# Performance work log

Hardware: AMD Instinct MI355X
Metric: run time of the kernel (lower is better)

Reference implementation:

```python
import jax, jax.numpy as jnp
import numpy as np
from jax import lax

COND, PRED, DH, NOUT = 64, 32, 128, 1
M, LQ, N, LR = 8, 256, 64, 512


def setup_inputs() -> dict:
    key = jax.random.key(0)
    ks = jax.random.split(key, 8)
    g = lambda k, sh, s=0.05: jax.random.normal(k, sh, jnp.float32) * s
    return {
        "query": jax.random.normal(ks[0], (M, LQ), jnp.float32),
        "ref": jax.random.normal(ks[1], (N, LR), jnp.float32),
        "q_weight": g(ks[2], (DH, 1, COND)),
        "q_bias": jnp.zeros((DH,), jnp.float32),
        "k_weight": g(ks[3], (DH, 1, COND)),
        "k_bias": jnp.zeros((DH,), jnp.float32),
        "v_weight": g(ks[4], (DH, 1, PRED), 0.1),
        "v_bias": jnp.zeros((DH,), jnp.float32),
        "m_weight": jnp.full((NOUT, 1, COND), 1.0 / COND, jnp.float32),
        "m_bias": jnp.zeros((NOUT,), jnp.float32),
        "o_weight": g(ks[5], (NOUT * PRED, DH), 0.1),
        "o_bias": jnp.zeros((NOUT * PRED,), jnp.float32),
        "m_key": g(ks[6], (1, 1, DH), 1.0),
    }


DN = ('NCH', 'OIH', 'NCH')


def _minmax_conv(x, w, b, offset=None, scale=None):
    # x: [B,1,L], w: [H,1,k] -> y: [B,H,W]. Each length-k window is min-max
    # normalized before the conv contraction. Since offset/scale are constant
    # per window: conv((x-off)/sc) = (conv(x) - off*sum(w)) / sc.
    k = w.shape[-1]
    if offset is None:
        offset = lax.reduce_window(x, jnp.inf, lax.min, (1, 1, k), (1, 1, 1), 'VALID')
    if scale is None:
        mx = lax.reduce_window(x, -jnp.inf, lax.max, (1, 1, k), (1, 1, 1), 'VALID')
        scale = mx - offset
        scale = jnp.where(scale == 0.0, 1.0, scale)
    raw = lax.conv_general_dilated(x, w, (1,), 'VALID', dimension_numbers=DN)
    wsum = w.sum(axis=(1, 2))
    y = (raw - offset * wsum[None, :, None]) / scale + b[None, :, None]
    return y, offset, scale


def reference(query, ref, q_weight, q_bias, k_weight, k_bias, v_weight, v_bias,
              m_weight, m_bias, o_weight, o_bias, m_key):
    cond, pred = q_weight.shape[-1], v_weight.shape[-1]
    # ---- query encoding ----
    q_in = jnp.cumsum(query, axis=1)[:, None, :]
    q, q_off, q_scale = _minmax_conv(q_in, q_weight, q_bias)
    q = q.transpose(0, 2, 1)                   # [M,Q,H]
    Qn = q.shape[1]
    q_scale_t = q_scale.transpose(0, 2, 1)     # [M,Q,1]
    qp = jnp.pad(query, ((0, 0), (cond - 1, 0)))[:, None, :]
    mc = lax.conv_general_dilated(qp, m_weight, (1,), 'VALID', dimension_numbers=DN)
    mc = mc + m_bias[None, :, None]
    mc = mc[..., cond - pred:]                 # [M,NOUT,Q+pred-1]
    widx = jnp.arange(pred)[:, None] + jnp.arange(Qn)[None, :]
    mwin = mc[..., widx]                       # [M,NOUT,pred,Q]
    m = mwin.reshape(mwin.shape[0], -1, Qn).transpose(0, 2, 1)  # [M,Q,NOUT*pred]
    m = m / q_scale_t
    # ---- key / value encoding ----
    k_in = jnp.cumsum(ref, axis=1)[:, None, :-pred]
    k, k_off, k_scale = _minmax_conv(k_in, k_weight, k_bias)
    k = k.transpose(0, 2, 1)                   # [N,K,H]
    v_in = ref[:, None, cond:]
    v, _, _ = _minmax_conv(v_in, v_weight, v_bias,
                           offset=jnp.zeros_like(k_off), scale=k_scale)
    v = v.transpose(0, 2, 1)                   # [N,K,H]
    # ---- scores ----
    full_score = jnp.einsum('mqh,nkh->mqkn', q, k)           # [M,Q,K,N]
    m_score = jnp.sum(q * m_key, axis=-1, keepdims=True)     # [M,Q,1]
    # ---- semi-hard attention: top-1 window per reference series ----
    ref_score = full_score.max(axis=2)         # [M,Q,N]
    max_idx = full_score.argmax(axis=2)        # [M,Q,N]
    n_ids = jnp.arange(v.shape[0])[None, None, :]
    sel_v = v[n_ids, max_idx]                  # [M,Q,N,H]
    sel_v = sel_v @ o_weight.T + o_bias        # [M,Q,N,D]
    scores = jax.nn.softmax(jnp.concatenate([ref_score, m_score], axis=-1), axis=-1)
    rs, ms = scores[..., :-1], scores[..., -1:]
    p = jnp.einsum('mqn,mqnd->mqd', rs, sel_v) + ms * m      # [M,Q,D]
    return p * q_scale_t
```

## Files before the change

kernel.cpp:

```cpp
#include <hip/hip_runtime.h>
#include <cmath>

#define M_B   8
#define LQ    256
#define N_B   64
#define LR    512
#define COND  64
#define PRED  32
#define DH    128
#define QN    193
#define KN    417
#define QPAD  256
#define KPAD  448
#define QROWS 1544
#define QGRPS 49

typedef _Float16 half8 __attribute__((ext_vector_type(8)));
typedef float f32x16 __attribute__((ext_vector_type(16)));

__device__ __forceinline__ f32x16 mfma_f16(half8 a, half8 b, f32x16 c) {
    return __builtin_amdgcn_mfma_f32_32x32x16_f16(a, b, c, 0, 0, 0);
}
__device__ __forceinline__ f32x16 zero16() {
    f32x16 z;
    #pragma unroll
    for (int i = 0; i < 16; i++) z[i] = 0.f;
    return z;
}

#define GLOAD_LDS16(g, l) __builtin_amdgcn_global_load_lds( \
    (const __attribute__((address_space(1))) void*)(g), \
    (__attribute__((address_space(3))) void*)(l), 16, 0, 0)

#define PIN_V(x) asm volatile("" : "+v"(x))

__launch_bounds__(256, 2)
__global__ void kA_feat(const float* __restrict__ query, const float* __restrict__ ref,
                        const float* __restrict__ qw, const float* __restrict__ qb,
                        const float* __restrict__ kw, const float* __restrict__ kb,
                        const float* __restrict__ vw, const float* __restrict__ vb,
                        float* __restrict__ q_scale, float* __restrict__ qfeat,
                        _Float16* __restrict__ qg,
                        _Float16* __restrict__ kg, float* __restrict__ vfeat) {
    __shared__ float x[512];
    __shared__ float buf[128 * 65];
    const int t = threadIdx.x;
    const int kl = t & 63;
    const int hq = __builtin_amdgcn_readfirstlane(t >> 6);

    if (blockIdx.x < 448) {
        const int n = blockIdx.x / 7, chunk = blockIdx.x % 7;
        x[t] = ref[n * 512 + t];
        x[t + 256] = ref[n * 512 + t + 256];
        __syncthreads();

        const int kp = chunk * 64 + kl;
        const bool vkp = kp < KN;
        float csw[64];
        float run = 0.f, mn = 0.f, mx = 0.f;
        csw[0] = 0.f;
        #pragma unroll
        for (int j = 1; j < 64; j++) {
            run += x[kp + j];
            csw[j] = run;
            mn = fminf(mn, run);
            mx = fmaxf(mx, run);
        }
        float scv = mx - mn; if (scv == 0.f) scv = 1.f;
        const float inv = 1.f / scv;
        #pragma unroll
        for (int j = 0; j < 64; j++) { csw[j] -= mn; PIN_V(csw[j]); }

        for (int hh = 0; hh < 32; hh++) {
            const int h = hq * 32 + hh;
            const float* wrow = kw + h * 64;
            float a0 = 0.f, a1 = 0.f, a2 = 0.f, a3 = 0.f;
            #pragma unroll
            for (int j = 0; j < 64; j += 4) {
                a0 = fmaf(wrow[j],     csw[j],     a0);
                a1 = fmaf(wrow[j + 1], csw[j + 1], a1);
                a2 = fmaf(wrow[j + 2], csw[j + 2], a2);
                a3 = fmaf(wrow[j + 3], csw[j + 3], a3);
            }
            float kraw = (a0 + a1) + (a2 + a3);
            float kval = vkp ? kraw * inv + kb[h] : 0.f;
            buf[h * 65 + (kl ^ (h >> 3))] = kval;
        }
        __syncthreads();
        {
            const size_t nb = ((size_t)n * KPAD + chunk * 64) * 256;
            #pragma unroll
            for (int r = 0; r < 8; r++) {
                int task = r * 256 + t;
                int kp_l = task >> 5, g = task & 31;
                int cb = g & 15, lo = g >> 4;
                half8 hv;
                #pragma unroll
                for (int jj = 0; jj < 8; jj++) {
                    float v = buf[(cb * 8 + jj) * 65 + (kp_l ^ cb)];
                    _Float16 hi = (_Float16)v;
                    hv[jj] = lo ? (_Float16)((v - (float)hi) * 1024.0f) : hi;
                }
                *(half8*)&kg[nb + (size_t)kp_l * 256 + ((size_t)(g ^ (kp_l & 31)) << 3)] = hv;
            }
        }
        __syncthreads();
        float refw[32];
        #pragma unroll
        for (int j = 0; j < 32; j++) {
            int ri = 64 + kp + j;
            refw[j] = (ri < 512) ? x[ri] : 0.f;
            PIN_V(refw[j]);
        }
        for (int hh = 0; hh < 32; hh++) {
            const int h = hq * 32 + hh;
            const float* vrow = vw + h * 32;
            float b0 = 0.f, b1 = 0.f;
            #pragma unroll
            for (int j = 0; j < 32; j += 2) {
                b0 = fmaf(vrow[j],     refw[j],     b0);
                b1 = fmaf(vrow[j + 1], refw[j + 1], b1);
            }
            float vval = vkp ? (b0 + b1) * inv + vb[h] : 0.f;
            buf[h * 65 + (kl ^ (h >> 3))] = vval;
        }
        __syncthreads();
        {
            const size_t vb0 = ((size_t)n * KPAD + chunk * 64) * 128;
            #pragma unroll
            for (int r = 0; r < 8; r++) {
                int idx = r * 256 + t;
                int kp_l = idx >> 5, c4 = idx & 31;
                float4 o;
                o.x = buf[(c4 * 4 + 0) * 65 + (kp_l ^ ((c4 * 4 + 0) >> 3))];
                o.y = buf[(c4 * 4 + 1) * 65 + (kp_l ^ ((c4 * 4 + 1) >> 3))];
                o.z = buf[(c4 * 4 + 2) * 65 + (kp_l ^ ((c4 * 4 + 2) >> 3))];
                o.w = buf[(c4 * 4 + 3) * 65 + (kp_l ^ ((c4 * 4 + 3) >> 3))];
                *(float4*)&vfeat[vb0 + (size_t)kp_l * 128 + c4 * 4] = o;
            }
        }
    } else {
        const int id = blockIdx.x - 448;
        const int m = id >> 2, qc = id & 3;
        x[t] = query[m * 256 + t];
        __syncthreads();

        const int qpos = qc * 64 + kl;
        const bool vq = qpos < QN;
        const int base = vq ? qpos : (QN - 1);
        float csw[64];
        float run = 0.f, mn = 0.f, mx = 0.f;
        csw[0] = 0.f;
        #pragma unroll
        for (int j = 1; j < 64; j++) {
            run += x[base + j];
            csw[j] = run;
            mn = fminf(mn, run);
            mx = fmaxf(mx, run);
        }
        float sc = mx - mn; if (sc == 0.f) sc = 1.f;
        const float inv = 1.f / sc;
        if (t < 64) q_scale[m * QPAD + qpos] = vq ? sc : 1.f;
        #pragma unroll
        for (int j = 0; j < 64; j++) { csw[j] -= mn; PIN_V(csw[j]); }

        for (int hh = 0; hh < 32; hh++) {
            const int h = hq * 32 + hh;
            const float* wrow = qw + h * 64;
            float a0 = 0.f, a1 = 0.f, a2 = 0.f, a3 = 0.f;
            #pragma unroll
            for (int j = 0; j < 64; j += 4) {
                a0 = fmaf(wrow[j],     csw[j],     a0);
                a1 = fmaf(wrow[j + 1], csw[j + 1], a1);
                a2 = fmaf(wrow[j + 2], csw[j + 2], a2);
                a3 = fmaf(wrow[j + 3], csw[j + 3], a3);
            }
            float raw = (a0 + a1) + (a2 + a3);
            float val = vq ? raw * inv + qb[h] : 0.f;
            buf[h * 65 + (kl ^ (h >> 3))] = val;
        }
        __syncthreads();
        const size_t qb0 = ((size_t)m * QPAD + qc * 64) * 128;
        #pragma unroll
        for (int r = 0; r < 8; r++) {
            int idx = r * 256 + t;
            int qp_l = idx >> 5, c4 = idx & 31;
            float4 o;
            o.x = buf[(c4 * 4 + 0) * 65 + (qp_l ^ ((c4 * 4 + 0) >> 3))];
            o.y = buf[(c4 * 4 + 1) * 65 + (qp_l ^ ((c4 * 4 + 1) >> 3))];
            o.z = buf[(c4 * 4 + 2) * 65 + (qp_l ^ ((c4 * 4 + 2) >> 3))];
            o.w = buf[(c4 * 4 + 3) * 65 + (qp_l ^ ((c4 * 4 + 3) >> 3))];
            *(float4*)&qfeat[qb0 + (size_t)qp_l * 128 + c4 * 4] = o;
        }
        #pragma unroll
        for (int r = 0; r < 8; r++) {
            int idx = r * 256 + t;
            int qp_l = idx >> 5, g = idx & 31;
            int c = g >> 2, kh = (g >> 1) & 1, lo = g & 1;
            int qp2 = qc * 64 + qp_l;
            if (qp2 < QN) {
                half8 hv;
                #pragma unroll
                for (int jj = 0; jj < 8; jj++) {
                    int h = c * 16 + kh * 8 + jj;
                    float v = buf[h * 65 + (qp_l ^ (h >> 3))];
                    _Float16 hi = (_Float16)v;
                    hv[jj] = lo ? (_Float16)((v - (float)hi) * 1024.0f) : hi;
                }
                int prow = m * QN + qp2;
                int grp = prow >> 5;
                size_t fb = (size_t)(grp * 16 + c * 2 + lo);
                *(half8*)&qg[fb * 512 + (size_t)(kh * 32 + (prow & 31)) * 8] = hv;
            }
        }
    }
}

__launch_bounds__(256, 3)
__global__ void k3_score(const _Float16* __restrict__ qg, const _Float16* __restrict__ kg,
                         float* __restrict__ bscore, int* __restrict__ bidx) {
    __shared__ _Float16 Kbuf[2][32 * 256];
    const int blk = blockIdx.x;
    const int n = blk & 63, qt = blk >> 6;
    const int t = threadIdx.x, w = t >> 6, l = t & 63;
    const int lrow = l & 31, khalf = l >> 5;

    const int grp = qt * 4 + w;
    half8 qf[8][2];
    #pragma unroll
    for (int c = 0; c < 8; c++)
        #pragma unroll
        for (int h = 0; h < 2; h++)
            qf[c][h] = ((const half8*)qg)[(size_t)(grp * 16 + c * 2 + h) * 64 + l];

    const _Float16* ksrc = kg + (size_t)n * KPAD * 256;

    float best[16];
    int bestkt[16];
    #pragma unroll
    for (int g = 0; g < 16; g++) { best[g] = -INFINITY; bestkt[g] = 0; }

    #pragma unroll
    for (int rd = 0; rd < 4; rd++) {
        int e = (rd * 4 + w) * 512 + l * 8;
        GLOAD_LDS16(ksrc + e, &Kbuf[0][0] + e);
    }

    for (int kt = 0; kt < 14; kt++) {
        __syncthreads();
        if (kt < 13) {
            const _Float16* src = ksrc + (size_t)(kt + 1) * (32 * 256);
            _Float16* dst = &Kbuf[(kt + 1) & 1][0];
            #pragma unroll
            for (int rd = 0; rd < 4; rd++) {
                int e = (rd * 4 + w) * 512 + l * 8;
                GLOAD_LDS16(src + e, dst + e);
            }
        }
        const _Float16* krow = &Kbuf[kt & 1][0] + lrow * 256;
        f32x16 accH = zero16(), accL = zero16();
        half8 bh = *(const half8*)(krow + ((khalf ^ lrow) * 8));
        half8 bl = *(const half8*)(krow + (((16 + khalf) ^ lrow) * 8));
        #pragma unroll
        for (int c = 0; c < 8; c++) {
            half8 nbh, nbl;
            if (c < 7) {
                nbh = *(const half8*)(krow + ((((c + 1) * 2 + khalf) ^ lrow) * 8));
                nbl = *(const half8*)(krow + (((16 + (c + 1) * 2 + khalf) ^ lrow) * 8));
            }
            accH = mfma_f16(qf[c][0], bh, accH);
            accL = mfma_f16(qf[c][0], bl, accL);
            accL = mfma_f16(qf[c][1], bh, accL);
            bh = nbh; bl = nbl;
        }
        const int kp = kt * 32 + lrow;
        const bool valid = kp < KN;
        #pragma unroll
        for (int g = 0; g < 16; g++) {
            float sv = fmaf(accL[g], 0.0009765625f, accH[g]);
            if (valid && (sv > best[g])) { best[g] = sv; bestkt[g] = kt; }
        }
    }

    #pragma unroll
    for (int g = 0; g < 16; g++) {
        float sv = best[g];
        int kp = bestkt[g] * 32 + lrow;
        for (int msk = 1; msk < 32; msk <<= 1) {
            float os = __shfl_xor(sv, msk, 64);
            int okp = __shfl_xor(kp, msk, 64);
            if (os > sv || (os == sv && okp < kp)) { sv = os; kp = okp; }
        }
        if (lrow == 0) {
            int row = (g & 3) + 8 * (g >> 2) + 4 * khalf;
            int mq = grp * 32 + row;
            if (mq < QROWS) {
                bscore[(size_t)mq * 64 + n] = sv;
                bidx[(size_t)mq * 64 + n] = kp;
            }
        }
    }
}

__global__ void k4_out(const float* __restrict__ query,
                       const float* __restrict__ qfeat, const float* __restrict__ vfeat,
                       const float* __restrict__ bscore, const int* __restrict__ bidx,
                       const float* __restrict__ q_scale,
                       const float* __restrict__ mw, const float* __restrict__ mb,
                       const float* __restrict__ mkey,
                       const float* __restrict__ ow, const float* __restrict__ ob,
                       float* __restrict__ out) {
    __shared__ float pS[4][128];
    const int t = threadIdx.x, wv = t >> 6, l = t & 63;
    const int j = blockIdx.x;
    const int m = j / QN, qpos = j - m * QN;
    const int mq = m * QPAD + qpos;

    float s = bscore[(size_t)j * 64 + l];
    int idx = bidx[(size_t)j * 64 + l];
    float msv = qfeat[(size_t)mq * 128 + l] * mkey[l]
              + qfeat[(size_t)mq * 128 + 64 + l] * mkey[64 + l];
    #pragma unroll
    for (int msk = 1; msk < 64; msk <<= 1) msv += __shfl_xor(msv, msk, 64);
    float mx = s;
    #pragma unroll
    for (int msk = 1; msk < 64; msk <<= 1) mx = fmaxf(mx, __shfl_xor(mx, msk, 64));
    mx = fmaxf(mx, msv);
    float e = expf(s - mx);
    float sum = e;
    #pragma unroll
    for (int msk = 1; msk < 64; msk <<= 1) sum += __shfl_xor(sum, msk, 64);
    float ems = expf(msv - mx);
    float inv = 1.f / (sum + ems);
    float rs = e * inv, msw = ems * inv;

    float ax = 0.f, ay = 0.f;
    #pragma unroll
    for (int k = 0; k < 16; k++) {
        int nn = wv * 16 + k;
        float r = __shfl(rs, nn, 64);
        int  id = __shfl(idx, nn, 64);
        const float2 v = *(const float2*)&vfeat[((size_t)nn * KPAD + id) * 128 + 2 * l];
        ax = fmaf(r, v.x, ax);
        ay = fmaf(r, v.y, ay);
    }
    pS[wv][2 * l] = ax; pS[wv][2 * l + 1] = ay;
    __syncthreads();
    if (t < 128) pS[0][t] = (pS[0][t] + pS[1][t]) + (pS[2][t] + pS[3][t]);
    __syncthreads();
    if (wv == 0 && l < 32) {
        float p = 0.f;
        #pragma unroll
        for (int h4 = 0; h4 < 32; h4++) {
            const float4 wv4 = *(const float4*)&pS[0][h4 * 4];
            const float4 o4 = *(const float4*)&ow[l * 128 + h4 * 4];
            p += wv4.x * o4.x + wv4.y * o4.y + wv4.z * o4.z + wv4.w * o4.w;
        }
        p += (1.f - msw) * ob[l];
        float mcv = mb[0];
        const int tpos = 32 + qpos + l;
        for (int jj = 0; jj < 64; jj++) {
            int qi = tpos + jj - 63;
            if (qi >= 0) mcv = fmaf(mw[jj], query[m * 256 + qi], mcv);
        }
        float outv = q_scale[mq] * p + msw * mcv;
        out[(size_t)j * 32 + l] = outv;
    }
}

extern "C" void kernel_launch(void* const* d_in, const int* in_sizes, int n_in,
                              void* d_out, int out_size, void* d_ws, size_t ws_size,
                              hipStream_t stream) {
    const float* query = (const float*)d_in[0];
    const float* ref   = (const float*)d_in[1];
    const float* qw    = (const float*)d_in[2];
    const float* qb    = (const float*)d_in[3];
    const float* kw    = (const float*)d_in[4];
    const float* kb    = (const float*)d_in[5];
    const float* vw    = (const float*)d_in[6];
    const float* vb    = (const float*)d_in[7];
    const float* mw    = (const float*)d_in[8];
    const float* mb    = (const float*)d_in[9];
    const float* ow    = (const float*)d_in[10];
    const float* ob    = (const float*)d_in[11];
    const float* mkey  = (const float*)d_in[12];
    float* out = (float*)d_out;

    float* ws = (float*)d_ws;
    float* q_scale = ws;
    float* qfeat   = ws + 2048;
    float* bscore  = ws + 264192;
    int*   bidx    = (int*)(ws + 395264);
    _Float16* qg   = (_Float16*)(ws + 526336);
    _Float16* kg   = (_Float16*)(ws + 788480);
    float* vfeat   = ws + 4458496;

    hipLaunchKernelGGL(kA_feat, dim3(480), dim3(256), 0, stream,
                       query, ref, qw, qb, kw, kb, vw, vb,
                       q_scale, qfeat, qg, kg, vfeat);
    hipLaunchKernelGGL(k3_score, dim3(832), dim3(256), 0, stream,
                       qg, kg, bscore, bidx);
    hipLaunchKernelGGL(k4_out, dim3(1544), dim3(256), 0, stream,
                       query, qfeat, vfeat, bscore, bidx, q_scale, mw, mb, mkey, ow, ob, out);
}
```

Measured before the change: 199.9 us.

## Process two reference series per block in score kernel to reuse query fragments

After: 199.1 us. About the same (-0.4%).

```diff
diff --git a/kernel.cpp b/kernel.cpp
--- a/kernel.cpp
+++ b/kernel.cpp
@@ -216,12 +216,13 @@
     }
 }
 
-__launch_bounds__(256, 3)
+__launch_bounds__(256, 2)
 __global__ void k3_score(const _Float16* __restrict__ qg, const _Float16* __restrict__ kg,
                          float* __restrict__ bscore, int* __restrict__ bidx) {
-    __shared__ _Float16 Kbuf[2][32 * 256];
+    __shared__ _Float16 Kbuf[2][2][32 * 256];
     const int blk = blockIdx.x;
-    const int n = blk & 63, qt = blk >> 6;
+    const int np = blk & 31, qt = blk >> 5;
+    const int n0 = np * 2;
     const int t = threadIdx.x, w = t >> 6, l = t & 63;
     const int lrow = l & 31, khalf = l >> 5;
 
@@ -233,70 +234,107 @@
         for (int h = 0; h < 2; h++)
             qf[c][h] = ((const half8*)qg)[(size_t)(grp * 16 + c * 2 + h) * 64 + l];
 
-    const _Float16* ksrc = kg + (size_t)n * KPAD * 256;
-
-    float best[16];
-    int bestkt[16];
-    #pragma unroll
-    for (int g = 0; g < 16; g++) { best[g] = -INFINITY; bestkt[g] = 0; }
+    const _Float16* ksrc0 = kg + (size_t)n0 * KPAD * 256;
+    const _Float16* ksrc1 = ksrc0 + (size_t)KPAD * 256;
+
+    float best0[16], best1[16];
+    unsigned bkt0[2] = {0u, 0u}, bkt1[2] = {0u, 0u};
+    #pragma unroll
+    for (int g = 0; g < 16; g++) { best0[g] = -INFINITY; best1[g] = -INFINITY; }
 
     #pragma unroll
     for (int rd = 0; rd < 4; rd++) {
         int e = (rd * 4 + w) * 512 + l * 8;
-        GLOAD_LDS16(ksrc + e, &Kbuf[0][0] + e);
+        GLOAD_LDS16(ksrc0 + e, &Kbuf[0][0][0] + e);
+        GLOAD_LDS16(ksrc1 + e, &Kbuf[0][1][0] + e);
     }
 
     for (int kt = 0; kt < 14; kt++) {
         __syncthreads();
         if (kt < 13) {
-            const _Float16* src = ksrc + (size_t)(kt + 1) * (32 * 256);
-            _Float16* dst = &Kbuf[(kt + 1) & 1][0];
+            const size_t off = (size_t)(kt + 1) * (32 * 256);
+            _Float16* dst0 = &Kbuf[(kt + 1) & 1][0][0];
+            _Float16* dst1 = &Kbuf[(kt + 1) & 1][1][0];
             #pragma unroll
             for (int rd = 0; rd < 4; rd++) {
                 int e = (rd * 4 + w) * 512 + l * 8;
-                GLOAD_LDS16(src + e, dst + e);
-            }
-        }
-        const _Float16* krow = &Kbuf[kt & 1][0] + lrow * 256;
-        f32x16 accH = zero16(), accL = zero16();
-        half8 bh = *(const half8*)(krow + ((khalf ^ lrow) * 8));
-        half8 bl = *(const half8*)(krow + (((16 + khalf) ^ lrow) * 8));
+                GLOAD_LDS16(ksrc0 + off + e, dst0 + e);
+                GLOAD_LDS16(ksrc1 + off + e, dst1 + e);
+            }
+        }
+        const _Float16* krow0 = &Kbuf[kt & 1][0][0] + lrow * 256;
+        const _Float16* krow1 = &Kbuf[kt & 1][1][0] + lrow * 256;
+        f32x16 accH0 = zero16(), accL0 = zero16();
+        f32x16 accH1 = zero16(), accL1 = zero16();
+        half8 bh0 = *(const half8*)(krow0 + ((khalf ^ lrow) * 8));
+        half8 bl0 = *(const half8*)(krow0 + (((16 + khalf) ^ lrow) * 8));
+        half8 bh1 = *(const half8*)(krow1 + ((khalf ^ lrow) * 8));
+        half8 bl1 = *(const half8*)(krow1 + (((16 + khalf) ^ lrow) * 8));
         #pragma unroll
         for (int c = 0; c < 8; c++) {
-            half8 nbh, nbl;
+            half8 nbh0, nbl0, nbh1, nbl1;
             if (c < 7) {
-                nbh = *(const half8*)(krow + ((((c + 1) * 2 + khalf) ^ lrow) * 8));
-                nbl = *(const half8*)(krow + (((16 + (c + 1) * 2 + khalf) ^ lrow) * 8));
-            }
-            accH = mfma_f16(qf[c][0], bh, accH);
-            accL = mfma_f16(qf[c][0], bl, accL);
-            accL = mfma_f16(qf[c][1], bh, accL);
-            bh = nbh; bl = nbl;
+                const int oh = (((c + 1) * 2 + khalf) ^ lrow) * 8;
+                const int ol = (((16 + (c + 1) * 2 + khalf)) ^ lrow) * 8;
+                nbh0 = *(const half8*)(krow0 + oh);
+                nbl0 = *(const half8*)(krow0 + ol);
+                nbh1 = *(const half8*)(krow1 + oh);
+                nbl1 = *(const half8*)(krow1 + ol);
+            }
+            accH0 = mfma_f16(qf[c][0], bh0, accH0);
+            accH1 = mfma_f16(qf[c][0], bh1, accH1);
+            accL0 = mfma_f16(qf[c][0], bl0, accL0);
+            accL1 = mfma_f16(qf[c][0], bl1, accL1);
+            accL0 = mfma_f16(qf[c][1], bh0, accL0);
+            accL1 = mfma_f16(qf[c][1], bh1, accL1);
+            bh0 = nbh0; bl0 = nbl0; bh1 = nbh1; bl1 = nbl1;
         }
         const int kp = kt * 32 + lrow;
         const bool valid = kp < KN;
         #pragma unroll
         for (int g = 0; g < 16; g++) {
-            float sv = fmaf(accL[g], 0.0009765625f, accH[g]);
-            if (valid && (sv > best[g])) { best[g] = sv; bestkt[g] = kt; }
+            const unsigned sh = (unsigned)(g & 7) * 4u;
+            float sv0 = fmaf(accL0[g], 0.0009765625f, accH0[g]);
+            if (valid && (sv0 > best0[g])) {
+                best0[g] = sv0;
+                bkt0[g >> 3] = (bkt0[g >> 3] & ~(0xFu << sh)) | ((unsigned)kt << sh);
+            }
+            float sv1 = fmaf(accL1[g], 0.0009765625f, accH1[g]);
+            if (valid && (sv1 > best1[g])) {
+                best1[g] = sv1;
+                bkt1[g >> 3] = (bkt1[g >> 3] & ~(0xFu << sh)) | ((unsigned)kt << sh);
+            }
         }
     }
 
     #pragma unroll
     for (int g = 0; g < 16; g++) {
-        float sv = best[g];
-        int kp = bestkt[g] * 32 + lrow;
-        for (int msk = 1; msk < 32; msk <<= 1) {
-            float os = __shfl_xor(sv, msk, 64);
-            int okp = __shfl_xor(kp, msk, 64);
-            if (os > sv || (os == sv && okp < kp)) { sv = os; kp = okp; }
-        }
-        if (lrow == 0) {
-            int row = (g & 3) + 8 * (g >> 2) + 4 * khalf;
-            int mq = grp * 32 + row;
-            if (mq < QROWS) {
-                bscore[(size_t)mq * 64 + n] = sv;
-                bidx[(size_t)mq * 64 + n] = kp;
+        const int row = (g & 3) + 8 * (g >> 2) + 4 * khalf;
+        const int mq = grp * 32 + row;
+        {
+            float sv = best0[g];
+            int kp = (int)((bkt0[g >> 3] >> ((g & 7) * 4)) & 0xFu) * 32 + lrow;
+            for (int msk = 1; msk < 32; msk <<= 1) {
+                float os = __shfl_xor(sv, msk, 64);
+                int okp = __shfl_xor(kp, msk, 64);
+                if (os > sv || (os == sv && okp < kp)) { sv = os; kp = okp; }
+            }
+            if (lrow == 0 && mq < QROWS) {
+                bscore[(size_t)mq * 64 + n0] = sv;
+                bidx[(size_t)mq * 64 + n0] = kp;
+            }
+        }
+        {
+            float sv = best1[g];
+            int kp = (int)((bkt1[g >> 3] >> ((g & 7) * 4)) & 0xFu) * 32 + lrow;
+            for (int msk = 1; msk < 32; msk <<= 1) {
+                float os = __shfl_xor(sv, msk, 64);
+                int okp = __shfl_xor(kp, msk, 64);
+                if (os > sv || (os == sv && okp < kp)) { sv = os; kp = okp; }
+            }
+            if (lrow == 0 && mq < QROWS) {
+                bscore[(size_t)mq * 64 + n0 + 1] = sv;
+                bidx[(size_t)mq * 64 + n0 + 1] = kp;
             }
         }
     }
@@ -398,7 +436,7 @@
     hipLaunchKernelGGL(kA_feat, dim3(480), dim3(256), 0, stream,
                        query, ref, qw, qb, kw, kb, vw, vb,
                        q_scale, qfeat, qg, kg, vfeat);
-    hipLaunchKernelGGL(k3_score, dim3(832), dim3(256), 0, stream,
+    hipLaunchKernelGGL(k3_score, dim3(416), dim3(256), 0, stream,
                        qg, kg, bscore, bidx);
     hipLaunchKernelGGL(k4_out, dim3(1544), dim3(256), 0, stream,
                        query, qfeat, vfeat, bscore, bidx, q_scale, mw, mb, mkey, ow, ob, out);
```
